# Performance work log

Measured on AMD Instinct MI355X. Metric: run time of the kernel, lower is better.

## Reference

```python
import jax, jax.numpy as jnp
import numpy as np

H = 2048        # hidden_size
E = 8           # num_experts
TOPK = 2
I = 1408        # moe_intermediate_size
IS = 5632       # shared_expert_intermediate_size
NORM_TOPK = True


def setup_inputs() -> dict:
    key = jax.random.key(0)
    ks = jax.random.split(key, 9)
    s = lambda k, shape: jax.random.normal(k, shape, dtype=jnp.float32) * (1.0 / np.sqrt(shape[-2] if len(shape) > 1 else shape[-1]))
    return {
        "hidden_states": jax.random.normal(ks[0], (1, 512, H), dtype=jnp.float32),
        "gate_w": jax.random.normal(ks[1], (E, H), dtype=jnp.float32) * 0.02,   # router Linear(H->E), no bias
        "w_gate": s(ks[2], (E, H, I)),   # expert gate_proj
        "w_up": s(ks[3], (E, H, I)),     # expert up_proj
        "w_down": s(ks[4], (E, I, H)),   # expert down_proj
        "sh_gate_w": s(ks[5], (H, IS)),  # shared expert gate_proj
        "sh_up_w": s(ks[6], (H, IS)),    # shared expert up_proj
        "sh_down_w": s(ks[7], (IS, H)),  # shared expert down_proj
        "shexp_gate_w": jax.random.normal(ks[8], (H, 1), dtype=jnp.float32) * 0.02,  # shared_expert_gate Linear(H->1)
    }


def reference(hidden_states, gate_w, w_gate, w_up, w_down,
              sh_gate_w, sh_up_w, sh_down_w, shexp_gate_w):
    B, S, _ = hidden_states.shape
    x = hidden_states.reshape(-1, H)                      # [T, H]
    T = x.shape[0]

    # --- router: softmax over all experts, then top-k (moe_gating_topk_softmax) ---
    router_logits = x @ gate_w.T                          # [T, E]
    probs = jax.nn.softmax(router_logits, axis=-1)
    routing_weights, selected_experts = jax.lax.top_k(probs, TOPK)  # [T, K]
    if NORM_TOPK:
        routing_weights = routing_weights / jnp.sum(routing_weights, axis=-1, keepdims=True)

    # dense combine weights: combine[t, e] = routing weight if expert e selected for token t else 0
    combine = jnp.zeros((T, E), dtype=x.dtype)
    combine = combine.at[jnp.arange(T)[:, None], selected_experts].set(routing_weights)

    # --- experts: SwiGLU MLP per expert, vectorized over E ---
    g = jnp.einsum('th,ehi->tei', x, w_gate)              # [T, E, I]
    u = jnp.einsum('th,ehi->tei', x, w_up)                # [T, E, I]
    h = jax.nn.silu(g) * u                                # [T, E, I]
    expert_out = jnp.einsum('tei,eih,te->th', h, w_down, combine)  # weighted scatter-add

    # --- shared expert with sigmoid gate ---
    sh = jax.nn.silu(x @ sh_gate_w) * (x @ sh_up_w)       # [T, IS]
    shared_out = (sh @ sh_down_w) * jax.nn.sigmoid(x @ shexp_gate_w)  # [T, H]

    out = (expert_out + shared_out).reshape(B, S, H)
    return (out, router_logits)
```

## Files before the change

### kernel.cpp

```cpp
#include <hip/hip_runtime.h>
#include <hip/hip_bf16.h>

#define NT  512
#define NH  2048
#define NE  8
#define NI  1408
#define NIS 5632

typedef __bf16 bf16x8 __attribute__((ext_vector_type(8)));
typedef float  f32x4  __attribute__((ext_vector_type(4)));

#define GLDS(gp, lp) __builtin_amdgcn_global_load_lds( \
    (const __attribute__((address_space(1))) void*)(gp), \
    (__attribute__((address_space(3))) void*)(lp), 16, 0, 0)

static constexpr size_t WS_XBF  = 0;
static constexpr size_t WS_SEL  = WS_XBF + (size_t)NT*NH*2;
static constexpr size_t WS_WTS  = WS_SEL + 4096;
static constexpr size_t WS_CNT  = WS_WTS + 4096;
static constexpr size_t WS_OFFE = WS_CNT + 32;
static constexpr size_t WS_TOK  = WS_OFFE + 32;
static constexpr size_t WS_PWT  = WS_TOK + 4096;
static constexpr size_t WS_SLOT = WS_PWT + 4096;
static constexpr size_t WS_G    = WS_SLOT + 4096;
static constexpr size_t WS_U    = WS_G   + (size_t)2*1024*NI*2;
static constexpr size_t WS_HBF  = WS_U   + (size_t)2*1024*NI*2;
static constexpr size_t WS_PAIR = WS_HBF + (size_t)1024*NI*2;
static constexpr size_t WS_SHG  = WS_PAIR+ (size_t)1024*NH*2;
static constexpr size_t WS_SHU  = WS_SHG + (size_t)2*NT*NIS*2;
static constexpr size_t WS_SHBF = WS_SHU + (size_t)2*NT*NIS*2;
static constexpr size_t WS_SHP  = WS_SHBF+ (size_t)NT*NIS*2;

__global__ void router_kernel(const float* __restrict__ x, const float* __restrict__ gw,
                              float* __restrict__ out_logits,
                              int* __restrict__ sel, float* __restrict__ wts)
{
    int w    = threadIdx.x >> 6;
    int lane = threadIdx.x & 63;
    int t    = blockIdx.x * 4 + w;
    int e    = lane & 7, c = lane >> 3;
    const float* xr = x  + (size_t)t * NH + c * 256;
    const float* gr = gw + (size_t)e * NH + c * 256;
    float acc = 0.f;
    #pragma unroll 8
    for (int it = 0; it < 64; ++it) {
        float4 xv = *(const float4*)(xr + it*4);
        float4 gv = *(const float4*)(gr + it*4);
        acc += xv.x*gv.x + xv.y*gv.y + xv.z*gv.z + xv.w*gv.w;
    }
    acc += __shfl_xor(acc, 8);
    acc += __shfl_xor(acc, 16);
    acc += __shfl_xor(acc, 32);
    if (lane < 8) out_logits[(size_t)t * NE + e] = acc;

    float l[8];
    #pragma unroll
    for (int j = 0; j < 8; ++j) l[j] = __shfl(acc, j);
    if (lane == 0) {
        int i1 = 0;
        #pragma unroll
        for (int j = 1; j < 8; ++j) if (l[j] > l[i1]) i1 = j;
        int i2 = -1;
        #pragma unroll
        for (int j = 0; j < 8; ++j) {
            if (j == i1) continue;
            if (i2 < 0 || l[j] > l[i2]) i2 = j;
        }
        float d  = expf(l[i2] - l[i1]);
        float w1 = 1.f / (1.f + d);
        float w2 = 1.f - w1;
        sel[2*t]   = i1;  sel[2*t+1] = i2;
        wts[2*t]   = w1;  wts[2*t+1] = w2;
    }
}

__global__ void bucket_kernel(const int* __restrict__ sel, const float* __restrict__ wts,
                              int* __restrict__ cnt, int* __restrict__ offe,
                              int* __restrict__ tok, float* __restrict__ pwt,
                              int* __restrict__ slot)
{
    int tid  = threadIdx.x;
    int wid  = tid >> 6;
    int lane = tid & 63;
    __shared__ int scnt[8], soff[8];

    unsigned long long masks[16];
    int total = 0;
    #pragma unroll
    for (int c = 0; c < 16; ++c) {
        int idx = c * 64 + lane;
        int s = sel[idx];
        unsigned long long m = __ballot(s == wid);
        masks[c] = m;
        total += __popcll(m);
    }
    if (lane == 0) { scnt[wid] = total; cnt[wid] = total; }
    __syncthreads();
    if (tid == 0) {
        int s = 0;
        #pragma unroll
        for (int j = 0; j < 8; ++j) { soff[j] = s; offe[j] = s; s += scnt[j]; }
    }
    __syncthreads();
    int pfx = soff[wid];
    unsigned long long below = (lane == 63) ? ~0ull >> 1 : ((1ull << lane) - 1);
    #pragma unroll
    for (int c = 0; c < 16; ++c) {
        int idx = c * 64 + lane;
        unsigned long long m = masks[c];
        if ((m >> lane) & 1ull) {
            int rank = pfx + (int)__popcll(m & below);
            tok[rank]  = idx >> 1;
            pwt[rank]  = wts[idx];
            slot[idx]  = rank;
        }
        pfx += (int)__popcll(m);
    }
}

__global__ void cast_kernel(const float* __restrict__ src, __bf16* __restrict__ dst, long long n)
{
    long long i = ((long long)blockIdx.x * blockDim.x + threadIdx.x) * 4;
    if (i >= n) return;
    float4 v = *(const float4*)(src + i);
    __bf16 o[4] = { (__bf16)v.x, (__bf16)v.y, (__bf16)v.z, (__bf16)v.w };
    *(uint2*)(dst + i) = *(const uint2*)o;
}

__global__ void silu_fused_kernel(const __bf16* __restrict__ g1, const __bf16* __restrict__ u1,
                                  __bf16* __restrict__ h1, long long n1, size_t ps1,
                                  const __bf16* __restrict__ g2, const __bf16* __restrict__ u2,
                                  __bf16* __restrict__ h2, long long n2, size_t ps2)
{
    long long i = ((long long)blockIdx.x * blockDim.x + threadIdx.x) * 8;
    const __bf16 *g, *u; __bf16* h; long long idx; size_t ps;
    if (i < n1)           { g = g1; u = u1; h = h1; idx = i;      ps = ps1; }
    else if (i < n1 + n2) { g = g2; u = u2; h = h2; idx = i - n1; ps = ps2; }
    else return;
    uint4 gv0 = *(const uint4*)(g + idx);
    uint4 gv1 = *(const uint4*)(g + idx + ps);
    uint4 uv0 = *(const uint4*)(u + idx);
    uint4 uv1 = *(const uint4*)(u + idx + ps);
    const __bf16* gp0 = (const __bf16*)&gv0;
    const __bf16* gp1 = (const __bf16*)&gv1;
    const __bf16* up0 = (const __bf16*)&uv0;
    const __bf16* up1 = (const __bf16*)&uv1;
    __bf16 o[8];
    #pragma unroll
    for (int j = 0; j < 8; ++j) {
        float xg = (float)gp0[j] + (float)gp1[j];
        float xu = (float)up0[j] + (float)up1[j];
        float y = xg / (1.f + __expf(-xg)) * xu;
        o[j] = (__bf16)y;
    }
    *(uint4*)(h + idx) = *(const uint4*)o;
}

template<int NK, int LDB, bool GATHER>
__device__ __forceinline__ void gemm_core(char* __restrict__ smem,
    const __bf16* __restrict__ A, int lda,
    const float* __restrict__ B,
    __bf16* __restrict__ C, int ldc,
    int rows, int base, const int* __restrict__ tok, int m0, int n0)
{
    const int tid  = threadIdx.x;
    const int lane = tid & 63;
    const int wid  = tid >> 6;
    const int wr   = wid >> 1, wc = wid & 1;

    const int rs0 = (wid*2 + 0)*16 + (lane >> 2);
    const int rs1 = (wid*2 + 1)*16 + (lane >> 2);
    const int cch = lane & 3;
    int ga0 = m0 + rs0, ga1 = m0 + rs1;
    int ar0, ar1;
    if (GATHER) {
        ar0 = tok[base + (ga0 < rows ? ga0 : 0)];
        ar1 = tok[base + (ga1 < rows ? ga1 : 0)];
    } else {
        ar0 = base + (ga0 < rows ? ga0 : 0);
        ar1 = base + (ga1 < rows ? ga1 : 0);
    }
    const __bf16* a0p = A + (size_t)ar0 * lda + (cch ^ (rs0 & 3)) * 8;
    const __bf16* a1p = A + (size_t)ar1 * lda + (cch ^ (rs1 & 3)) * 8;

#define AGLDS(slot, t)                                               \
    {                                                                \
        char* d0 = smem + (slot)*8192 + (wid*2 + 0)*1024;            \
        char* d1 = smem + (slot)*8192 + (wid*2 + 1)*1024;            \
        GLDS(a0p + (size_t)(t)*32, d0);                              \
        GLDS(a1p + (size_t)(t)*32, d1);                              \
    }

    const int cn4 = (tid & 31) * 4;
    const int kr4 = (tid >> 5) * 4;
    const int kck = kr4 >> 3;
    const int kh  = (kr4 >> 2) & 1;
    const float* bp = B + (size_t)kr4 * LDB + n0 + cn4;
    char* bbuf0 = smem + 24576;
    char* bbuf1 = smem + 32768;

#define BLOAD(R, t)                                                  \
    {                                                                \
        const float* bq = bp + (size_t)(t) * 32 * LDB;               \
        _Pragma("unroll")                                            \
        for (int j = 0; j < 4; ++j)                                  \
            R[j] = *(const float4*)(bq + (size_t)j * LDB);           \
    }

#define CONVERT(R, bbase)                                            \
    {                                                                \
        _Pragma("unroll")                                            \
        for (int c = 0; c < 4; ++c) {                                \
            __bf16 ob[4];                                            \
            _Pragma("unroll")                                        \
            for (int j = 0; j < 4; ++j)                              \
                ob[j] = (__bf16)(((const float*)(R))[j*4 + c]);      \
            int col = cn4 + c;                                       \
            *(uint2*)((bbase) + col*64 + ((kck ^ ((col>>1)&3)) * 16) + kh*8) = *(const uint2*)ob; \
        }                                                            \
    }

    const int fr = lane & 15, fq = lane >> 4;
    const int aoff = (wr*64 + fr)*64 + ((fq ^ (fr & 3)) * 16);
    const int boff = (wc*64 + fr)*64 + ((fq ^ ((fr >> 1) & 3)) * 16);

    f32x4 acc[4][4];
    #pragma unroll
    for (int i = 0; i < 4; ++i)
        #pragma unroll
        for (int j = 0; j < 4; ++j) acc[i][j] = f32x4{0.f,0.f,0.f,0.f};

#define MFMAS(slot, bbase)                                           \
    {                                                                \
        const char* Ab = smem + (slot)*8192;                         \
        bf16x8 af[4], bfr[4];                                        \
        _Pragma("unroll")                                            \
        for (int m = 0; m < 4; ++m) af[m]  = *(const bf16x8*)(Ab + aoff + m*1024); \
        _Pragma("unroll")                                            \
        for (int n = 0; n < 4; ++n) bfr[n] = *(const bf16x8*)((bbase) + boff + n*1024); \
        __builtin_amdgcn_s_setprio(1);                               \
        _Pragma("unroll")                                            \
        for (int m = 0; m < 4; ++m)                                  \
            _Pragma("unroll")                                        \
            for (int n = 0; n < 4; ++n)                              \
                acc[m][n] = __builtin_amdgcn_mfma_f32_16x16x32_bf16(af[m], bfr[n], acc[m][n], 0, 0, 0); \
        __builtin_amdgcn_s_setprio(0);                               \
    }

    float4 b0[4], b1[4];

    BLOAD(b0, 0); AGLDS(0, 0);
    BLOAD(b1, 1); AGLDS(1, 1);
    asm volatile("s_waitcnt vmcnt(6)" ::: "memory");
    CONVERT(b0, bbuf0);
    asm volatile("s_waitcnt lgkmcnt(0)" ::: "memory");
    __builtin_amdgcn_s_barrier();

    int sA = 0, sB = 1, sC = 2;
    #pragma unroll 1
    for (int t = 0; t < NK; t += 2) {
        if (t + 2 < NK) { BLOAD(b0, t + 2); AGLDS(sC, t + 2); }
        __builtin_amdgcn_sched_barrier(0);
        MFMAS(sA, bbuf0);
        __builtin_amdgcn_sched_barrier(0);
        if (t + 2 < NK) asm volatile("s_waitcnt vmcnt(6)" ::: "memory");
        else            asm volatile("s_waitcnt vmcnt(0)" ::: "memory");
        CONVERT(b1, bbuf1);
        asm volatile("s_waitcnt lgkmcnt(0)" ::: "memory");
        __builtin_amdgcn_s_barrier();

        if (t + 3 < NK) { BLOAD(b1, t + 3); AGLDS(sA, t + 3); }
        __builtin_amdgcn_sched_barrier(0);
        MFMAS(sB, bbuf1);
        __builtin_amdgcn_sched_barrier(0);
        if (t + 2 < NK) {
            if (t + 3 < NK) asm volatile("s_waitcnt vmcnt(6)" ::: "memory");
            else            asm volatile("s_waitcnt vmcnt(0)" ::: "memory");
            CONVERT(b0, bbuf0);
        }
        asm volatile("s_waitcnt lgkmcnt(0)" ::: "memory");
        __builtin_amdgcn_s_barrier();

        int tmp = sA; sA = sC; sC = sB; sB = tmp;
    }
#undef AGLDS
#undef BLOAD
#undef CONVERT
#undef MFMAS

    __bf16* ep = (__bf16*)(smem + wid * 9216);
    #pragma unroll
    for (int m = 0; m < 4; ++m)
        #pragma unroll
        for (int n = 0; n < 4; ++n)
            #pragma unroll
            for (int q = 0; q < 4; ++q)
                ep[(m*16 + fq*4 + q)*72 + n*16 + fr] = (__bf16)acc[m][n][q];

    const int grow = m0 + wr*64 + lane;
    if (grow < rows) {
        __bf16* cp = C + (size_t)(base + grow) * ldc + n0 + wc*64;
        const __bf16* rp = ep + lane * 72;
        #pragma unroll
        for (int j = 0; j < 8; ++j)
            *(uint4*)(cp + j*8) = *(const uint4*)(rp + j*8);
    }
}

__launch_bounds__(256, 3)
__global__ void gemm_p1(const __bf16* __restrict__ xbf,
                        const float* __restrict__ w_gate, const float* __restrict__ w_up,
                        const float* __restrict__ sh_gate, const float* __restrict__ sh_up,
                        __bf16* __restrict__ gbuf, __bf16* __restrict__ ubuf,
                        __bf16* __restrict__ shg, __bf16* __restrict__ shu,
                        const int* __restrict__ cnt, const int* __restrict__ offe,
                        const int* __restrict__ tok)
{
    __shared__ alignas(16) char smem[40960];
    int g = blockIdx.x;
    int x = g & 7;
    int j = g >> 3;
    if (j < 176) {
        int gu = j / 88;
        int r  = j % 88;
        int k2 = r / 44;
        int rr = r % 44;
        int n  = rr % 11;
        int m  = rr / 11;
        int rows = cnt[x], base = offe[x];
        int m0 = m * 128; if (m0 >= rows) return;
        const float* B = (gu == 0 ? w_gate : w_up) + (size_t)x * NH * NI + (size_t)k2 * 1024 * NI;
        __bf16* C = (gu == 0 ? gbuf : ubuf) + (size_t)k2 * 1024 * NI;
        gemm_core<32, NI, true>(smem, xbf + k2 * 1024, NH, B, C, NI,
                                rows, base, tok, m0, n * 128);
    } else {
        int s = j - 176;
        int z = s / 48;
        int rem = s % 48;
        int k2 = rem / 24;
        int rem2 = rem % 24;
        int i = rem2 >> 2;
        int m = rem2 & 3;
        int n = x + 8 * i;
        if (n >= 44) return;
        const float* B = (z == 0 ? sh_gate : sh_up) + (size_t)k2 * 1024 * NIS;
        __bf16* C = (z == 0 ? shg : shu) + (size_t)k2 * NT * NIS;
        gemm_core<32, NIS, false>(smem, xbf + k2 * 1024, NH, B, C, NIS,
                                  NT, 0, nullptr, m * 128, n * 128);
    }
}

__launch_bounds__(256, 3)
__global__ void gemm_p3(const __bf16* __restrict__ hbf, const __bf16* __restrict__ shbf,
                        const float* __restrict__ w_down, const float* __restrict__ sh_down,
                        __bf16* __restrict__ pair, __bf16* __restrict__ shp,
                        const int* __restrict__ cnt, const int* __restrict__ offe)
{
    __shared__ alignas(16) char smem[40960];
    int g = blockIdx.x;
    int x = g & 7;
    int j = g >> 3;
    if (j < 64) {
        int n = j % 16;
        int m = j / 16;
        int rows = cnt[x], base = offe[x];
        int m0 = m * 128; if (m0 >= rows) return;
        gemm_core<NI/32, NH, false>(smem, hbf, NI, w_down + (size_t)x * NI * NH,
                                    pair, NH, rows, base, nullptr, m0, n * 128);
    } else {
        int s = j - 64;
        int q = s >> 3;
        int rem = s & 7;
        int i = rem >> 2;
        int m = rem & 3;
        int n = x + 8 * i;
        gemm_core<NI/32, NH, false>(smem, shbf + q * NI, NIS,
                                    sh_down + (size_t)q * NI * NH,
                                    shp + (size_t)q * NT * NH, NH,
                                    NT, 0, nullptr, m * 128, n * 128);
    }
}

__global__ void combine_kernel(const float* __restrict__ x, const float* __restrict__ shexp_w,
                               const __bf16* __restrict__ shp, const __bf16* __restrict__ pair_out,
                               const int* __restrict__ slot, const float* __restrict__ wts,
                               float* __restrict__ out)
{
    int t = blockIdx.x;
    int tid = threadIdx.x;
    const float* xr = x + (size_t)t * NH;

    float p = 0.f;
    #pragma unroll
    for (int j = 0; j < 8; ++j) {
        int k = tid * 8 + j;
        p += xr[k] * shexp_w[k];
    }
    __shared__ float red[256];
    red[tid] = p;
    __syncthreads();
    for (int s = 128; s > 0; s >>= 1) {
        if (tid < s) red[tid] += red[tid + s];
        __syncthreads();
    }
    float sig = 1.f / (1.f + expf(-red[0]));

    int   s0 = slot[2*t],   s1 = slot[2*t+1];
    float w0 = wts[2*t],    w1 = wts[2*t+1];
    const __bf16* pr0 = pair_out + (size_t)s0 * NH;
    const __bf16* pr1 = pair_out + (size_t)s1 * NH;
    const __bf16* sd  = shp + (size_t)t * NH;
    float* orow = out + (size_t)t * NH;
    const size_t PS = (size_t)NT * NH;
    for (int n = tid; n < NH; n += 256) {
        float sdv = (float)sd[n] + (float)sd[n + PS] + (float)sd[n + 2*PS] + (float)sd[n + 3*PS];
        orow[n] = sdv * sig + w0 * (float)pr0[n] + w1 * (float)pr1[n];
    }
}

extern "C" void kernel_launch(void* const* d_in, const int* in_sizes, int n_in,
                              void* d_out, int out_size, void* d_ws, size_t ws_size,
                              hipStream_t stream)
{
    const float* x       = (const float*)d_in[0];
    const float* gate_w  = (const float*)d_in[1];
    const float* w_gate  = (const float*)d_in[2];
    const float* w_up    = (const float*)d_in[3];
    const float* w_down  = (const float*)d_in[4];
    const float* sh_gate = (const float*)d_in[5];
    const float* sh_up   = (const float*)d_in[6];
    const float* sh_down = (const float*)d_in[7];
    const float* shexp_g = (const float*)d_in[8];

    float* out        = (float*)d_out;
    float* out_logits = out + (size_t)NT * NH;

    char* ws = (char*)d_ws;
    __bf16* xbf  = (__bf16*)(ws + WS_XBF);
    int*    sel  = (int*)  (ws + WS_SEL);
    float*  wts  = (float*)(ws + WS_WTS);
    int*    cnt  = (int*)  (ws + WS_CNT);
    int*    offe = (int*)  (ws + WS_OFFE);
    int*    tok  = (int*)  (ws + WS_TOK);
    float*  pwt  = (float*)(ws + WS_PWT);
    int*    slot = (int*)  (ws + WS_SLOT);
    __bf16* gbuf = (__bf16*)(ws + WS_G);
    __bf16* ubuf = (__bf16*)(ws + WS_U);
    __bf16* hbf  = (__bf16*)(ws + WS_HBF);
    __bf16* pair = (__bf16*)(ws + WS_PAIR);
    __bf16* shg  = (__bf16*)(ws + WS_SHG);
    __bf16* shu  = (__bf16*)(ws + WS_SHU);
    __bf16* shbf = (__bf16*)(ws + WS_SHBF);
    __bf16* shp  = (__bf16*)(ws + WS_SHP);
    (void)pwt; (void)in_sizes; (void)n_in; (void)out_size; (void)ws_size;

    router_kernel<<<dim3(128), dim3(256), 0, stream>>>(x, gate_w, out_logits, sel, wts);
    bucket_kernel<<<dim3(1), dim3(512), 0, stream>>>(sel, wts, cnt, offe, tok, pwt, slot);
    cast_kernel<<<dim3(1024), dim3(256), 0, stream>>>(x, xbf, (long long)NT * NH);

    gemm_p1<<<dim3(2176), dim3(256), 0, stream>>>(
        xbf, w_gate, w_up, sh_gate, sh_up, gbuf, ubuf, shg, shu, cnt, offe, tok);

    silu_fused_kernel<<<dim3(2112), dim3(256), 0, stream>>>(
        gbuf, ubuf, hbf, (long long)1024 * NI, (size_t)1024 * NI,
        shg, shu, shbf, (long long)NT * NIS, (size_t)NT * NIS);

    gemm_p3<<<dim3(768), dim3(256), 0, stream>>>(
        hbf, shbf, w_down, sh_down, pair, shp, cnt, offe);

    combine_kernel<<<dim3(NT), dim3(256), 0, stream>>>(
        x, shexp_g, shp, pair, slot, wts, out);
}
```

Measured before the change: 214.7 us.

## Split expert down-proj K in two, restructure B loading and pipeline

```diff
diff --git a/kernel.cpp b/kernel.cpp
--- a/kernel.cpp
+++ b/kernel.cpp
@@ -26,7 +26,7 @@
 static constexpr size_t WS_U    = WS_G   + (size_t)2*1024*NI*2;
 static constexpr size_t WS_HBF  = WS_U   + (size_t)2*1024*NI*2;
 static constexpr size_t WS_PAIR = WS_HBF + (size_t)1024*NI*2;
-static constexpr size_t WS_SHG  = WS_PAIR+ (size_t)1024*NH*2;
+static constexpr size_t WS_SHG  = WS_PAIR+ (size_t)2*1024*NH*2;
 static constexpr size_t WS_SHU  = WS_SHG + (size_t)2*NT*NIS*2;
 static constexpr size_t WS_SHBF = WS_SHU + (size_t)2*NT*NIS*2;
 static constexpr size_t WS_SHP  = WS_SHBF+ (size_t)NT*NIS*2;
@@ -191,33 +191,27 @@
         GLDS(a1p + (size_t)(t)*32, d1);                              \
     }
 
-    const int cn4 = (tid & 31) * 4;
-    const int kr4 = (tid >> 5) * 4;
-    const int kck = kr4 >> 3;
-    const int kh  = (kr4 >> 2) & 1;
-    const float* bp = B + (size_t)kr4 * LDB + n0 + cn4;
-    char* bbuf0 = smem + 24576;
-    char* bbuf1 = smem + 32768;
+    const int cn  = tid & 127;
+    const int ckh = tid >> 7;
+    const int csw = (cn >> 1) & 3;
+    const float* bp = B + (size_t)(ckh * 16) * LDB + n0 + cn;
+    char* bbuf0 = smem + 16384;
+    char* bbuf1 = smem + 24576;
 
 #define BLOAD(R, t)                                                  \
     {                                                                \
         const float* bq = bp + (size_t)(t) * 32 * LDB;               \
         _Pragma("unroll")                                            \
-        for (int j = 0; j < 4; ++j)                                  \
-            R[j] = *(const float4*)(bq + (size_t)j * LDB);           \
+        for (int j = 0; j < 16; ++j) R[j] = bq[(size_t)j * LDB];     \
     }
 
 #define CONVERT(R, bbase)                                            \
     {                                                                \
+        __bf16 ob[16];                                               \
         _Pragma("unroll")                                            \
-        for (int c = 0; c < 4; ++c) {                                \
-            __bf16 ob[4];                                            \
-            _Pragma("unroll")                                        \
-            for (int j = 0; j < 4; ++j)                              \
-                ob[j] = (__bf16)(((const float*)(R))[j*4 + c]);      \
-            int col = cn4 + c;                                       \
-            *(uint2*)((bbase) + col*64 + ((kck ^ ((col>>1)&3)) * 16) + kh*8) = *(const uint2*)ob; \
-        }                                                            \
+        for (int j = 0; j < 16; ++j) ob[j] = (__bf16)R[j];           \
+        *(uint4*)((bbase) + cn*64 + (((ckh*2 + 0) ^ csw) * 16)) = ((const uint4*)ob)[0]; \
+        *(uint4*)((bbase) + cn*64 + (((ckh*2 + 1) ^ csw) * 16)) = ((const uint4*)ob)[1]; \
     }
 
     const int fr = lane & 15, fq = lane >> 4;
@@ -247,41 +241,36 @@
         __builtin_amdgcn_s_setprio(0);                               \
     }
 
-    float4 b0[4], b1[4];
-
-    BLOAD(b0, 0); AGLDS(0, 0);
-    BLOAD(b1, 1); AGLDS(1, 1);
-    asm volatile("s_waitcnt vmcnt(6)" ::: "memory");
+    float b0[16], b1[16];
+
+    AGLDS(0, 0);
+    BLOAD(b0, 0);
+    BLOAD(b1, 1);
+    asm volatile("s_waitcnt vmcnt(16)" ::: "memory");
     CONVERT(b0, bbuf0);
     asm volatile("s_waitcnt lgkmcnt(0)" ::: "memory");
     __builtin_amdgcn_s_barrier();
 
-    int sA = 0, sB = 1, sC = 2;
     #pragma unroll 1
-    for (int t = 0; t < NK; t += 2) {
-        if (t + 2 < NK) { BLOAD(b0, t + 2); AGLDS(sC, t + 2); }
+    for (int t = 0; t < NK; ++t) {
+        if (t + 1 < NK) AGLDS((t + 1) & 1, t + 1);
+        if (t + 2 < NK) {
+            if (t & 1) { BLOAD(b1, t + 2); } else { BLOAD(b0, t + 2); }
+        }
         __builtin_amdgcn_sched_barrier(0);
-        MFMAS(sA, bbuf0);
-        __builtin_amdgcn_sched_barrier(0);
-        if (t + 2 < NK) asm volatile("s_waitcnt vmcnt(6)" ::: "memory");
-        else            asm volatile("s_waitcnt vmcnt(0)" ::: "memory");
-        CONVERT(b1, bbuf1);
-        asm volatile("s_waitcnt lgkmcnt(0)" ::: "memory");
-        __builtin_amdgcn_s_barrier();
-
-        if (t + 3 < NK) { BLOAD(b1, t + 3); AGLDS(sA, t + 3); }
-        __builtin_amdgcn_sched_barrier(0);
-        MFMAS(sB, bbuf1);
+        if (t & 1) { MFMAS(1, bbuf1); } else { MFMAS(0, bbuf0); }
         __builtin_amdgcn_sched_barrier(0);
         if (t + 2 < NK) {
-            if (t + 3 < NK) asm volatile("s_waitcnt vmcnt(6)" ::: "memory");
-            else            asm volatile("s_waitcnt vmcnt(0)" ::: "memory");
-            CONVERT(b0, bbuf0);
+            asm volatile("s_waitcnt vmcnt(18)" ::: "memory");
+            if (t & 1) { CONVERT(b0, bbuf0); } else { CONVERT(b1, bbuf1); }
+            asm volatile("s_waitcnt vmcnt(16)" ::: "memory");
+        } else if (t + 1 < NK) {
+            asm volatile("s_waitcnt vmcnt(2)" ::: "memory");
+            if (t & 1) { CONVERT(b0, bbuf0); } else { CONVERT(b1, bbuf1); }
+            asm volatile("s_waitcnt vmcnt(0)" ::: "memory");
         }
         asm volatile("s_waitcnt lgkmcnt(0)" ::: "memory");
         __builtin_amdgcn_s_barrier();
-
-        int tmp = sA; sA = sC; sC = sB; sB = tmp;
     }
 #undef AGLDS
 #undef BLOAD
@@ -316,7 +305,7 @@
                         const int* __restrict__ cnt, const int* __restrict__ offe,
                         const int* __restrict__ tok)
 {
-    __shared__ alignas(16) char smem[40960];
+    __shared__ alignas(16) char smem[36864];
     int g = blockIdx.x;
     int x = g & 7;
     int j = g >> 3;
@@ -356,28 +345,32 @@
                         __bf16* __restrict__ pair, __bf16* __restrict__ shp,
                         const int* __restrict__ cnt, const int* __restrict__ offe)
 {
-    __shared__ alignas(16) char smem[40960];
+    __shared__ alignas(16) char smem[36864];
     int g = blockIdx.x;
     int x = g & 7;
     int j = g >> 3;
-    if (j < 64) {
-        int n = j % 16;
-        int m = j / 16;
+    if (j < 128) {
+        int k2 = j >> 6;
+        int r  = j & 63;
+        int n  = r & 15;
+        int m  = r >> 4;
         int rows = cnt[x], base = offe[x];
         int m0 = m * 128; if (m0 >= rows) return;
-        gemm_core<NI/32, NH, false>(smem, hbf, NI, w_down + (size_t)x * NI * NH,
-                                    pair, NH, rows, base, nullptr, m0, n * 128);
+        gemm_core<22, NH, false>(smem, hbf + k2 * 704, NI,
+                                 w_down + (size_t)x * NI * NH + (size_t)k2 * 704 * NH,
+                                 pair + (size_t)k2 * 1024 * NH, NH,
+                                 rows, base, nullptr, m0, n * 128);
     } else {
-        int s = j - 64;
+        int s = j - 128;
         int q = s >> 3;
         int rem = s & 7;
         int i = rem >> 2;
         int m = rem & 3;
         int n = x + 8 * i;
-        gemm_core<NI/32, NH, false>(smem, shbf + q * NI, NIS,
-                                    sh_down + (size_t)q * NI * NH,
-                                    shp + (size_t)q * NT * NH, NH,
-                                    NT, 0, nullptr, m * 128, n * 128);
+        gemm_core<44, NH, false>(smem, shbf + q * NI, NIS,
+                                 sh_down + (size_t)q * NI * NH,
+                                 shp + (size_t)q * NT * NH, NH,
+                                 NT, 0, nullptr, m * 128, n * 128);
     }
 }
 
@@ -412,9 +405,12 @@
     const __bf16* sd  = shp + (size_t)t * NH;
     float* orow = out + (size_t)t * NH;
     const size_t PS = (size_t)NT * NH;
+    const size_t PP = (size_t)1024 * NH;
     for (int n = tid; n < NH; n += 256) {
         float sdv = (float)sd[n] + (float)sd[n + PS] + (float)sd[n + 2*PS] + (float)sd[n + 3*PS];
-        orow[n] = sdv * sig + w0 * (float)pr0[n] + w1 * (float)pr1[n];
+        float p0v = (float)pr0[n] + (float)pr0[n + PP];
+        float p1v = (float)pr1[n] + (float)pr1[n + PP];
+        orow[n] = sdv * sig + w0 * p0v + w1 * p1v;
     }
 }
 
@@ -465,7 +461,7 @@
         gbuf, ubuf, hbf, (long long)1024 * NI, (size_t)1024 * NI,
         shg, shu, shbf, (long long)NT * NIS, (size_t)NT * NIS);
 
-    gemm_p3<<<dim3(768), dim3(256), 0, stream>>>(
+    gemm_p3<<<dim3(1280), dim3(256), 0, stream>>>(
         hbf, shbf, w_down, sh_down, pair, shp, cnt, offe);
 
     combine_kernel<<<dim3(NT), dim3(256), 0, stream>>>(
```

New measurement: 654.6 us. 205% more time.
